# Performance work log

Measured on AMD Instinct MI355X. Metric: run time of the kernel, lower is better.

The kernel has to match this reference:

```python
import jax, jax.numpy as jnp
import numpy as np

N_NODES = 50000
N_EDGES = 600000
D = 128
R = 8


def setup_inputs() -> dict:
    key = jax.random.key(0)
    ks = jax.random.split(key, 10)
    return {
        "node_ids": jnp.arange(N_NODES, dtype=jnp.int32),
        "src": jax.random.randint(ks[0], (N_EDGES,), 0, N_NODES, dtype=jnp.int32),
        "dst": jax.random.randint(ks[1], (N_EDGES,), 0, N_NODES, dtype=jnp.int32),
        "etype": jax.random.randint(ks[2], (N_EDGES,), 0, R, dtype=jnp.int32),
        "emb": jax.random.normal(ks[3], (N_NODES, D), dtype=jnp.float32) * 0.02,
        "W1": jax.random.normal(ks[4], (R, D, D), dtype=jnp.float32) * 0.05,
        "Wself1": jax.random.normal(ks[5], (D, D), dtype=jnp.float32) * 0.05,
        "b1": jnp.zeros((D,), dtype=jnp.float32),
        "W2": jax.random.normal(ks[6], (R, D, D), dtype=jnp.float32) * 0.05,
        "Wself2": jax.random.normal(ks[7], (D, D), dtype=jnp.float32) * 0.05,
        "b2": jnp.zeros((D,), dtype=jnp.float32),
    }


def rgcn_layer(h, W, Wself, b, src, dst, etype, n_nodes):
    # relation-wise transform of all node features: [R, N, d_out]
    hr = jnp.einsum('nd,rdo->rno', h, W)
    # per-edge gather of (relation, src) -> message, then scatter-sum to dst
    msgs = hr[etype, src]                                   # [E, d_out]
    agg = jax.ops.segment_sum(msgs, dst, num_segments=n_nodes)
    # self-loop + bias (activation=None, feat_drop=0)
    return agg + h @ Wself + b


def reference(node_ids, src, dst, etype, emb, W1, Wself1, b1, W2, Wself2, b2):
    h0 = emb[node_ids]                                      # embedding lookup over all nodes
    h1 = rgcn_layer(h0, W1, Wself1, b1, src, dst, etype, emb.shape[0])
    h2 = rgcn_layer(h1, W2, Wself2, b2, src, dst, etype, emb.shape[0])
    return h2
```

## Files before the change

kernel.cpp:

```cpp
#include <hip/hip_runtime.h>
#include <hip/hip_bf16.h>

#define NN 50000
#define NE 600000
#define DD 128
#define NR 8
#define NB (NN * NR)
#define NCHUNK8 ((NB + 255) / 256)
#define PERT ((NCHUNK8 + 255) / 256)
#define CAPE 1024

typedef __attribute__((ext_vector_type(8))) short bf16x8;
typedef __attribute__((ext_vector_type(4))) float f32x4;

__device__ __forceinline__ unsigned short f2bf(float f) {
  __hip_bfloat16 h = __float2bfloat16(f);
  return *reinterpret_cast<unsigned short*>(&h);
}
__device__ __forceinline__ unsigned pk2(float lo, float hi) {
  return (unsigned)f2bf(lo) | ((unsigned)f2bf(hi) << 16);
}
__device__ __forceinline__ float bflo(unsigned u) { return __uint_as_float(u << 16); }
__device__ __forceinline__ float bfhi(unsigned u) { return __uint_as_float(u & 0xffff0000u); }

__global__ __launch_bounds__(128) void convw_kernel(
    const float* __restrict__ W1, const float* __restrict__ Ws1,
    const float* __restrict__ W2, const float* __restrict__ Ws2,
    unsigned short* __restrict__ WT)
{
  const int m = blockIdx.y, o = blockIdx.x, d = threadIdx.x;
  const float* src;
  if (m < 8)       src = W1 + (size_t)m * DD * DD;
  else if (m == 8) src = Ws1;
  else if (m < 17) src = W2 + (size_t)(m - 9) * DD * DD;
  else             src = Ws2;
  WT[(size_t)m * DD * DD + o * DD + d] = f2bf(src[(size_t)d * DD + o]);
}

__global__ __launch_bounds__(256) void convh_kernel(
    const float* __restrict__ emb, const int* __restrict__ ids,
    unsigned short* __restrict__ h)
{
  const int gid = blockIdx.x * 256 + threadIdx.x;
  if (gid >= NN * 16) return;
  const int row = gid >> 4;
  const int off = (gid & 15) * 8;
  const int srcRow = ids[row];
  const float* src = emb + (size_t)srcRow * DD + off;
  const float4 a = *reinterpret_cast<const float4*>(src);
  const float4 b = *reinterpret_cast<const float4*>(src + 4);
  uint4 u;
  u.x = pk2(a.x, a.y); u.y = pk2(a.z, a.w);
  u.z = pk2(b.x, b.y); u.w = pk2(b.z, b.w);
  *reinterpret_cast<uint4*>(h + (size_t)row * DD + off) = u;
}

__global__ __launch_bounds__(256) void hist_kernel(
    const int* __restrict__ dst, const int* __restrict__ et,
    int* __restrict__ deg)
{
  const int e = blockIdx.x * 256 + threadIdx.x;
  if (e < NE) atomicAdd(&deg[dst[e] * NR + et[e]], 1);
}

__global__ __launch_bounds__(256) void bsum_kernel(
    const int* __restrict__ deg, int* __restrict__ bsum)
{
  __shared__ int tmp[256];
  const int t = threadIdx.x;
  const int i = blockIdx.x * 256 + t;
  tmp[t] = (i < NB) ? deg[i] : 0;
  __syncthreads();
#pragma unroll
  for (int off = 128; off > 0; off >>= 1) {
    if (t < off) tmp[t] += tmp[t + off];
    __syncthreads();
  }
  if (t == 0) bsum[blockIdx.x] = tmp[0];
}

__global__ __launch_bounds__(256) void bscan_kernel(
    const int* __restrict__ bsum, int* __restrict__ bbase)
{
  __shared__ int tmp[256];
  const int t = threadIdx.x;
  const int b = t * PERT;
  const int e = min(b + PERT, NCHUNK8);
  int s = 0;
  for (int i = b; i < e; ++i) s += bsum[i];
  tmp[t] = s;
  __syncthreads();
#pragma unroll
  for (int off = 1; off < 256; off <<= 1) {
    const int x = (t >= off) ? tmp[t - off] : 0;
    __syncthreads();
    tmp[t] += x;
    __syncthreads();
  }
  int run = tmp[t] - s;
  for (int i = b; i < e; ++i) {
    const int v = bsum[i];
    bbase[i] = run;
    run += v;
  }
}

__global__ __launch_bounds__(256) void expand_kernel(
    int* deg, const int* __restrict__ bbase, int* __restrict__ offsets)
{
  __shared__ int tmp[256];
  const int t = threadIdx.x;
  const int i = blockIdx.x * 256 + t;
  const int v = (i < NB) ? deg[i] : 0;
  tmp[t] = v;
  __syncthreads();
#pragma unroll
  for (int off = 1; off < 256; off <<= 1) {
    const int x = (t >= off) ? tmp[t - off] : 0;
    __syncthreads();
    tmp[t] += x;
    __syncthreads();
  }
  const int base = bbase[blockIdx.x];
  const int excl = base + tmp[t] - v;
  if (i < NB) {
    offsets[i] = excl;
    deg[i] = excl;
    if (i == NB - 1) offsets[NB] = base + tmp[t];
  }
}

__global__ __launch_bounds__(256) void fill_kernel(
    const int* __restrict__ src, const int* __restrict__ dst,
    const int* __restrict__ et, int* __restrict__ cursor,
    int* __restrict__ eidx)
{
  const int e = blockIdx.x * 256 + threadIdx.x;
  if (e < NE) {
    const int pos = atomicAdd(&cursor[dst[e] * NR + et[e]], 1);
    eidx[pos] = src[e];
  }
}

__device__ __forceinline__ void gacc_row(
    const unsigned short* __restrict__ h, int idx, int g, float s[4][8])
{
  const unsigned short* hp = h + (size_t)idx * DD + g * 8;
#pragma unroll
  for (int ks = 0; ks < 4; ++ks) {
    const uint4 q = *reinterpret_cast<const uint4*>(hp + ks * 32);
    s[ks][0] += bflo(q.x); s[ks][1] += bfhi(q.x);
    s[ks][2] += bflo(q.y); s[ks][3] += bfhi(q.y);
    s[ks][4] += bflo(q.z); s[ks][5] += bfhi(q.z);
    s[ks][6] += bflo(q.w); s[ks][7] += bfhi(q.w);
  }
}

__device__ __forceinline__ void gather_frag_lds(
    const unsigned short* __restrict__ h,
    const int* __restrict__ eidx, const int* ldsE, int blockBeg,
    int beg, int end, int g, bf16x8* frag)
{
  float s[4][8];
#pragma unroll
  for (int ks = 0; ks < 4; ++ks)
#pragma unroll
    for (int j = 0; j < 8; ++j) s[ks][j] = 0.f;
  for (int i = beg; i < end; ++i) {
    const int li = i - blockBeg;
    const int idx = (li < CAPE) ? ldsE[li] : eidx[i];
    gacc_row(h, idx, g, s);
  }
#pragma unroll
  for (int ks = 0; ks < 4; ++ks) {
    uint4 u;
    u.x = pk2(s[ks][0], s[ks][1]);
    u.y = pk2(s[ks][2], s[ks][3]);
    u.z = pk2(s[ks][4], s[ks][5]);
    u.w = pk2(s[ks][6], s[ks][7]);
    frag[ks] = *reinterpret_cast<bf16x8*>(&u);
  }
}

template<int OUTF32>
__global__ __launch_bounds__(256, 4) void layer_kernel(
    const unsigned short* __restrict__ h,
    const int* __restrict__ off8, const int* __restrict__ eidx,
    const unsigned short* __restrict__ WTl,
    const float* __restrict__ bias,
    void* __restrict__ out)
{
  __shared__ __align__(16) char ldsW[2][DD * 64 * 2];
  __shared__ int ldsO[64 * NR + 1];
  __shared__ int ldsE[CAPE];

  const int tid = threadIdx.x;
  const int rowBase = blockIdx.x * 64;
  const int lane = tid & 63;
  const int w = tid >> 6;
  const int c = lane & 15;
  const int g = lane >> 4;
  const int n = rowBase + w * 16 + c;
  const int nld = (n < NN) ? n : (NN - 1);
  const int lnode = nld - rowBase;

  const int nNodes = (NN - rowBase < 64) ? (NN - rowBase) : 64;
  const int onum = nNodes * NR + 1;
  for (int i = tid; i < onum; i += 256) ldsO[i] = off8[rowBase * NR + i];
  __syncthreads();
  const int blockBeg = ldsO[0];
  const int blockCnt = ldsO[onum - 1] - blockBeg;
  const int stCnt = (blockCnt < CAPE) ? blockCnt : CAPE;
  for (int i = tid; i < stCnt; i += 256) ldsE[i] = eidx[blockBeg + i];

  int dstB[4], srcRel[4];
#pragma unroll
  for (int j = 0; j < 4; ++j) {
    const int i = tid + j * 256;
    const int o = i >> 3, slot = i & 7;
    dstB[j] = ((o << 7) | (slot << 4)) ^ ((o & 7) << 4);
    srcRel[j] = o * DD + slot * 8;
  }

  uint4 wreg[4];
#pragma unroll
  for (int j = 0; j < 4; ++j)
    wreg[j] = *reinterpret_cast<const uint4*>(WTl + srcRel[j]);
#pragma unroll
  for (int j = 0; j < 4; ++j)
    *reinterpret_cast<uint4*>(ldsW[0] + dstB[j]) = wreg[j];
  __syncthreads();

  bf16x8 fA[4], fB[4];
  gather_frag_lds(h, eidx, ldsE, blockBeg, ldsO[lnode * NR], ldsO[lnode * NR + 1], g, fA);

  f32x4 acc[8];
#pragma unroll
  for (int t = 0; t < 8; ++t) acc[t] = (f32x4){0.f, 0.f, 0.f, 0.f};

#define PH(P, CUR, NXT)                                                               \
  {                                                                                   \
    __syncthreads();                                                                  \
    if ((P) < 17) {                                                                   \
      const unsigned short* wsrc = WTl                                                \
          + (size_t)(((P) + 1) >> 1) * DD * DD + (((P) + 1) & 1) * 64;                \
      _Pragma("unroll")                                                               \
      for (int j = 0; j < 4; ++j)                                                     \
        wreg[j] = *reinterpret_cast<const uint4*>(wsrc + srcRel[j]);                  \
    }                                                                                 \
    int gb = 0, ge = 0;                                                               \
    if (((P) & 1) == 0 && ((P) >> 1) + 1 < NR) {                                      \
      const int lo = lnode * NR + ((P) >> 1) + 1;                                     \
      gb = ldsO[lo]; ge = ldsO[lo + 1];                                               \
    }                                                                                 \
    _Pragma("unroll")                                                                 \
    for (int kl = 0; kl < 2; ++kl) {                                                  \
      _Pragma("unroll")                                                               \
      for (int t = 0; t < 8; ++t) {                                                   \
        const int addr = (((t * 16 + c) << 7) + ((kl * 4 + g) << 4)) ^ ((c & 7) << 4); \
        bf16x8 a = *reinterpret_cast<const bf16x8*>(ldsW[(P) & 1] + addr);            \
        acc[t] = __builtin_amdgcn_mfma_f32_16x16x32_bf16(                             \
            a, CUR[((P) & 1) * 2 + kl], acc[t], 0, 0, 0);                             \
      }                                                                               \
    }                                                                                 \
    if (((P) & 1) == 0) {                                                             \
      if (((P) >> 1) + 1 < NR) {                                                      \
        gather_frag_lds(h, eidx, ldsE, blockBeg, gb, ge, g, NXT);                     \
      } else if (((P) >> 1) + 1 == NR) {                                              \
        _Pragma("unroll")                                                             \
        for (int ks = 0; ks < 4; ++ks)                                                \
          NXT[ks] = *reinterpret_cast<const bf16x8*>(                                 \
              h + (size_t)nld * DD + ks * 32 + g * 8);                                \
      }                                                                               \
    }                                                                                 \
    if ((P) < 17) {                                                                   \
      _Pragma("unroll")                                                               \
      for (int j = 0; j < 4; ++j)                                                     \
        *reinterpret_cast<uint4*>(ldsW[((P) + 1) & 1] + dstB[j]) = wreg[j];           \
    }                                                                                 \
  }

  PH(0, fA, fB)  PH(1, fA, fB)
  PH(2, fB, fA)  PH(3, fB, fA)
  PH(4, fA, fB)  PH(5, fA, fB)
  PH(6, fB, fA)  PH(7, fB, fA)
  PH(8, fA, fB)  PH(9, fA, fB)
  PH(10, fB, fA) PH(11, fB, fA)
  PH(12, fA, fB) PH(13, fA, fB)
  PH(14, fB, fA) PH(15, fB, fA)
  PH(16, fA, fB) PH(17, fA, fB)
#undef PH

  if (n >= NN) return;
  if (OUTF32) {
    float* dst = (float*)out + (size_t)n * DD;
#pragma unroll
    for (int t = 0; t < 8; ++t) {
      const int o0 = t * 16 + g * 4;
      const float4 bv = *reinterpret_cast<const float4*>(bias + o0);
      float4 o;
      o.x = acc[t][0] + bv.x; o.y = acc[t][1] + bv.y;
      o.z = acc[t][2] + bv.z; o.w = acc[t][3] + bv.w;
      *reinterpret_cast<float4*>(dst + o0) = o;
    }
  } else {
    unsigned short* dst = (unsigned short*)out + (size_t)n * DD;
#pragma unroll
    for (int t = 0; t < 8; ++t) {
      const int o0 = t * 16 + g * 4;
      const float4 bv = *reinterpret_cast<const float4*>(bias + o0);
      uint2 q;
      q.x = pk2(acc[t][0] + bv.x, acc[t][1] + bv.y);
      q.y = pk2(acc[t][2] + bv.z, acc[t][3] + bv.w);
      *reinterpret_cast<uint2*>(dst + o0) = q;
    }
  }
}

extern "C" void kernel_launch(void* const* d_in, const int* in_sizes, int n_in,
                              void* d_out, int out_size, void* d_ws, size_t ws_size,
                              hipStream_t stream) {
  const int*   node_ids = (const int*)d_in[0];
  const int*   src   = (const int*)d_in[1];
  const int*   dst   = (const int*)d_in[2];
  const int*   etype = (const int*)d_in[3];
  const float* emb   = (const float*)d_in[4];
  const float* W1    = (const float*)d_in[5];
  const float* Ws1   = (const float*)d_in[6];
  const float* b1    = (const float*)d_in[7];
  const float* W2    = (const float*)d_in[8];
  const float* Ws2   = (const float*)d_in[9];
  const float* b2    = (const float*)d_in[10];

  char* p = (char*)d_ws;
  unsigned short* h0 = (unsigned short*)p;  p += (size_t)NN * DD * 2;
  unsigned short* h1 = (unsigned short*)p;  p += (size_t)NN * DD * 2;
  unsigned short* WT = (unsigned short*)p;  p += (size_t)18 * DD * DD * 2;
  int* off8          = (int*)p;             p += (size_t)(NB + 1) * 4;
  int* deg8          = (int*)p;             p += (size_t)NB * 4;
  int* eidx          = (int*)p;             p += (size_t)NE * 4;
  int* bsum          = (int*)p;             p += (size_t)NCHUNK8 * 4;
  int* bbase         = (int*)p;

  const int eb = (NE + 255) / 256;
  const int tb = (NN + 63) / 64;

  convw_kernel<<<dim3(DD, 18), 128, 0, stream>>>(W1, Ws1, W2, Ws2, WT);
  convh_kernel<<<(NN * 16) / 256, 256, 0, stream>>>(emb, node_ids, h0);
  hipMemsetAsync(deg8, 0, (size_t)NB * 4, stream);
  hist_kernel<<<eb, 256, 0, stream>>>(dst, etype, deg8);
  bsum_kernel<<<NCHUNK8, 256, 0, stream>>>(deg8, bsum);
  bscan_kernel<<<1, 256, 0, stream>>>(bsum, bbase);
  expand_kernel<<<NCHUNK8, 256, 0, stream>>>(deg8, bbase, off8);
  fill_kernel<<<eb, 256, 0, stream>>>(src, dst, etype, deg8, eidx);

  layer_kernel<0><<<tb, 256, 0, stream>>>(h0, off8, eidx, WT, b1, h1);
  layer_kernel<1><<<tb, 256, 0, stream>>>(h1, off8, eidx, WT + (size_t)9 * DD * DD, b2, (float*)d_out);
}
```

Baseline: 235.4 us.

## Read weights directly from global/L2 in MFMA loop, drop LDS weight double-buffer

```diff
diff --git a/kernel.cpp b/kernel.cpp
--- a/kernel.cpp
+++ b/kernel.cpp
@@ -8,7 +8,7 @@
 #define NB (NN * NR)
 #define NCHUNK8 ((NB + 255) / 256)
 #define PERT ((NCHUNK8 + 255) / 256)
-#define CAPE 1024
+#define CAPE 4096
 
 typedef __attribute__((ext_vector_type(8))) short bf16x8;
 typedef __attribute__((ext_vector_type(4))) float f32x4;
@@ -23,18 +23,24 @@
 __device__ __forceinline__ float bflo(unsigned u) { return __uint_as_float(u << 16); }
 __device__ __forceinline__ float bfhi(unsigned u) { return __uint_as_float(u & 0xffff0000u); }
 
-__global__ __launch_bounds__(128) void convw_kernel(
+__global__ __launch_bounds__(256) void convw_kernel(
     const float* __restrict__ W1, const float* __restrict__ Ws1,
     const float* __restrict__ W2, const float* __restrict__ Ws2,
     unsigned short* __restrict__ WT)
 {
-  const int m = blockIdx.y, o = blockIdx.x, d = threadIdx.x;
+  __shared__ float tile[16][17];
+  const int m = blockIdx.y;
+  const int t8 = blockIdx.x;
+  const int d0 = (t8 >> 3) * 16, o0 = (t8 & 7) * 16;
   const float* src;
   if (m < 8)       src = W1 + (size_t)m * DD * DD;
   else if (m == 8) src = Ws1;
   else if (m < 17) src = W2 + (size_t)(m - 9) * DD * DD;
   else             src = Ws2;
-  WT[(size_t)m * DD * DD + o * DD + d] = f2bf(src[(size_t)d * DD + o]);
+  const int tx = threadIdx.x & 15, ty = threadIdx.x >> 4;
+  tile[ty][tx] = src[(size_t)(d0 + ty) * DD + o0 + tx];
+  __syncthreads();
+  WT[(size_t)m * DD * DD + (o0 + ty) * DD + d0 + tx] = f2bf(tile[tx][ty]);
 }
 
 __global__ __launch_bounds__(256) void convh_kernel(
@@ -142,20 +148,6 @@
   }
 }
 
-__device__ __forceinline__ void gacc_row(
-    const unsigned short* __restrict__ h, int idx, int g, float s[4][8])
-{
-  const unsigned short* hp = h + (size_t)idx * DD + g * 8;
-#pragma unroll
-  for (int ks = 0; ks < 4; ++ks) {
-    const uint4 q = *reinterpret_cast<const uint4*>(hp + ks * 32);
-    s[ks][0] += bflo(q.x); s[ks][1] += bfhi(q.x);
-    s[ks][2] += bflo(q.y); s[ks][3] += bfhi(q.y);
-    s[ks][4] += bflo(q.z); s[ks][5] += bfhi(q.z);
-    s[ks][6] += bflo(q.w); s[ks][7] += bfhi(q.w);
-  }
-}
-
 __device__ __forceinline__ void gather_frag_lds(
     const unsigned short* __restrict__ h,
     const int* __restrict__ eidx, const int* ldsE, int blockBeg,
@@ -169,7 +161,15 @@
   for (int i = beg; i < end; ++i) {
     const int li = i - blockBeg;
     const int idx = (li < CAPE) ? ldsE[li] : eidx[i];
-    gacc_row(h, idx, g, s);
+    const unsigned short* hp = h + (size_t)idx * DD + g * 8;
+#pragma unroll
+    for (int ks = 0; ks < 4; ++ks) {
+      const uint4 q = *reinterpret_cast<const uint4*>(hp + ks * 32);
+      s[ks][0] += bflo(q.x); s[ks][1] += bfhi(q.x);
+      s[ks][2] += bflo(q.y); s[ks][3] += bfhi(q.y);
+      s[ks][4] += bflo(q.z); s[ks][5] += bfhi(q.z);
+      s[ks][6] += bflo(q.w); s[ks][7] += bfhi(q.w);
+    }
   }
 #pragma unroll
   for (int ks = 0; ks < 4; ++ks) {
@@ -183,14 +183,13 @@
 }
 
 template<int OUTF32>
-__global__ __launch_bounds__(256, 4) void layer_kernel(
+__global__ __launch_bounds__(256, 3) void layer_kernel(
     const unsigned short* __restrict__ h,
     const int* __restrict__ off8, const int* __restrict__ eidx,
     const unsigned short* __restrict__ WTl,
     const float* __restrict__ bias,
     void* __restrict__ out)
 {
-  __shared__ __align__(16) char ldsW[2][DD * 64 * 2];
   __shared__ int ldsO[64 * NR + 1];
   __shared__ int ldsE[CAPE];
 
@@ -212,84 +211,42 @@
   const int blockCnt = ldsO[onum - 1] - blockBeg;
   const int stCnt = (blockCnt < CAPE) ? blockCnt : CAPE;
   for (int i = tid; i < stCnt; i += 256) ldsE[i] = eidx[blockBeg + i];
-
-  int dstB[4], srcRel[4];
-#pragma unroll
-  for (int j = 0; j < 4; ++j) {
-    const int i = tid + j * 256;
-    const int o = i >> 3, slot = i & 7;
-    dstB[j] = ((o << 7) | (slot << 4)) ^ ((o & 7) << 4);
-    srcRel[j] = o * DD + slot * 8;
-  }
-
-  uint4 wreg[4];
-#pragma unroll
-  for (int j = 0; j < 4; ++j)
-    wreg[j] = *reinterpret_cast<const uint4*>(WTl + srcRel[j]);
-#pragma unroll
-  for (int j = 0; j < 4; ++j)
-    *reinterpret_cast<uint4*>(ldsW[0] + dstB[j]) = wreg[j];
-  __syncthreads();
+  __syncthreads();
+
+  f32x4 acc[8];
+#pragma unroll
+  for (int t = 0; t < 8; ++t) acc[t] = (f32x4){0.f, 0.f, 0.f, 0.f};
 
   bf16x8 fA[4], fB[4];
   gather_frag_lds(h, eidx, ldsE, blockBeg, ldsO[lnode * NR], ldsO[lnode * NR + 1], g, fA);
 
-  f32x4 acc[8];
-#pragma unroll
-  for (int t = 0; t < 8; ++t) acc[t] = (f32x4){0.f, 0.f, 0.f, 0.f};
-
-#define PH(P, CUR, NXT)                                                               \
+#define GS(R, CUR, NXT)                                                               \
   {                                                                                   \
-    __syncthreads();                                                                  \
-    if ((P) < 17) {                                                                   \
-      const unsigned short* wsrc = WTl                                                \
-          + (size_t)(((P) + 1) >> 1) * DD * DD + (((P) + 1) & 1) * 64;                \
+    if ((R) + 1 < NR) {                                                               \
+      gather_frag_lds(h, eidx, ldsE, blockBeg,                                        \
+                      ldsO[lnode * NR + (R) + 1], ldsO[lnode * NR + (R) + 2], g, NXT);\
+    } else if ((R) + 1 == NR) {                                                       \
       _Pragma("unroll")                                                               \
-      for (int j = 0; j < 4; ++j)                                                     \
-        wreg[j] = *reinterpret_cast<const uint4*>(wsrc + srcRel[j]);                  \
+      for (int ks = 0; ks < 4; ++ks)                                                  \
+        NXT[ks] = *reinterpret_cast<const bf16x8*>(                                   \
+            h + (size_t)nld * DD + ks * 32 + g * 8);                                  \
     }                                                                                 \
-    int gb = 0, ge = 0;                                                               \
-    if (((P) & 1) == 0 && ((P) >> 1) + 1 < NR) {                                      \
-      const int lo = lnode * NR + ((P) >> 1) + 1;                                     \
-      gb = ldsO[lo]; ge = ldsO[lo + 1];                                               \
-    }                                                                                 \
+    const unsigned short* wr = WTl + (size_t)(R) * DD * DD;                           \
     _Pragma("unroll")                                                                 \
-    for (int kl = 0; kl < 2; ++kl) {                                                  \
+    for (int t = 0; t < 8; ++t) {                                                     \
+      const unsigned short* ar = wr + (size_t)(t * 16 + c) * DD + g * 8;              \
       _Pragma("unroll")                                                               \
-      for (int t = 0; t < 8; ++t) {                                                   \
-        const int addr = (((t * 16 + c) << 7) + ((kl * 4 + g) << 4)) ^ ((c & 7) << 4); \
-        bf16x8 a = *reinterpret_cast<const bf16x8*>(ldsW[(P) & 1] + addr);            \
-        acc[t] = __builtin_amdgcn_mfma_f32_16x16x32_bf16(                             \
-            a, CUR[((P) & 1) * 2 + kl], acc[t], 0, 0, 0);                             \
+      for (int ks = 0; ks < 4; ++ks) {                                                \
+        bf16x8 a = *reinterpret_cast<const bf16x8*>(ar + ks * 32);                    \
+        acc[t] = __builtin_amdgcn_mfma_f32_16x16x32_bf16(a, CUR[ks], acc[t], 0, 0, 0);\
       }                                                                               \
     }                                                                                 \
-    if (((P) & 1) == 0) {                                                             \
-      if (((P) >> 1) + 1 < NR) {                                                      \
-        gather_frag_lds(h, eidx, ldsE, blockBeg, gb, ge, g, NXT);                     \
-      } else if (((P) >> 1) + 1 == NR) {                                              \
-        _Pragma("unroll")                                                             \
-        for (int ks = 0; ks < 4; ++ks)                                                \
-          NXT[ks] = *reinterpret_cast<const bf16x8*>(                                 \
-              h + (size_t)nld * DD + ks * 32 + g * 8);                                \
-      }                                                                               \
-    }                                                                                 \
-    if ((P) < 17) {                                                                   \
-      _Pragma("unroll")                                                               \
-      for (int j = 0; j < 4; ++j)                                                     \
-        *reinterpret_cast<uint4*>(ldsW[((P) + 1) & 1] + dstB[j]) = wreg[j];           \
-    }                                                                                 \
-  }
-
-  PH(0, fA, fB)  PH(1, fA, fB)
-  PH(2, fB, fA)  PH(3, fB, fA)
-  PH(4, fA, fB)  PH(5, fA, fB)
-  PH(6, fB, fA)  PH(7, fB, fA)
-  PH(8, fA, fB)  PH(9, fA, fB)
-  PH(10, fB, fA) PH(11, fB, fA)
-  PH(12, fA, fB) PH(13, fA, fB)
-  PH(14, fB, fA) PH(15, fB, fA)
-  PH(16, fA, fB) PH(17, fA, fB)
-#undef PH
+  }
+
+  GS(0, fA, fB) GS(1, fB, fA) GS(2, fA, fB) GS(3, fB, fA)
+  GS(4, fA, fB) GS(5, fB, fA) GS(6, fA, fB) GS(7, fB, fA)
+  GS(8, fA, fB)
+#undef GS
 
   if (n >= NN) return;
   if (OUTF32) {
@@ -345,7 +302,7 @@
   const int eb = (NE + 255) / 256;
   const int tb = (NN + 63) / 64;
 
-  convw_kernel<<<dim3(DD, 18), 128, 0, stream>>>(W1, Ws1, W2, Ws2, WT);
+  convw_kernel<<<dim3(64, 18), 256, 0, stream>>>(W1, Ws1, W2, Ws2, WT);
   convh_kernel<<<(NN * 16) / 256, 256, 0, stream>>>(emb, node_ids, h0);
   hipMemsetAsync(deg8, 0, (size_t)NB * 4, stream);
   hist_kernel<<<eb, 256, 0, stream>>>(dst, etype, deg8);
```

Result: slower. 490.0 us (+108.2%).
